# Performance work log

Hardware: AMD Instinct MI355X
Metric: run time of the kernel (lower is better)

The kernel has to match this reference:

```python
import jax, jax.numpy as jnp
import numpy as np


def setup_inputs() -> dict:
    key = jax.random.key(0)
    k1, k2 = jax.random.split(key)
    hidden_states = jax.random.normal(k1, (4, 4096, 2048), dtype=jnp.float32)
    routing_params = jax.random.normal(k2, (3, 2048), dtype=jnp.float32)
    return {"hidden_states": hidden_states, "routing_params": routing_params}


def reference(hidden_states, routing_params):
    B, S, H = hidden_states.shape
    D = routing_params.shape[0]  # max_recursion_depth
    k = max(1, int(S * (1.0 / D)))  # top-k tokens selected per step

    depth_assignments = jnp.zeros((B, S), dtype=jnp.int32)
    active_mask = jnp.ones((B, S), dtype=bool)
    rows = jnp.arange(B)[:, None]  # [B,1] row indices for scatter
    scores_list = []

    for r in range(D):  # small fixed depth loop
        raw = jnp.einsum('bsh,h->bs', hidden_states, routing_params[r])
        sc = jax.nn.sigmoid(raw)
        scores_list.append(sc)
        masked = jnp.where(active_mask, sc, -jnp.inf)
        _, top_idx = jax.lax.top_k(masked, k)  # [B,k]
        depth_assignments = depth_assignments.at[rows, top_idx].set(r + 1)
        step_mask = jnp.zeros((B, S), dtype=bool).at[rows, top_idx].set(True)
        active_mask = active_mask & step_mask

    depth_assignments = jnp.where(depth_assignments == 0, 1, depth_assignments)

    # balancing loss: note the original applies sigmoid AGAIN to the already-sigmoided scores
    probs = jax.nn.sigmoid(jnp.stack(scores_list, axis=-1)).mean(axis=(0, 1))  # [D]
    target = jnp.ones_like(probs) / D
    # F.kl_div(probs.log(), target, reduction='batchmean') with input of size D
    balancing_loss = jnp.sum(target * (jnp.log(target) - jnp.log(probs))) / D

    masks = jnp.stack([jnp.ones_like(active_mask) if r == 0 else active_mask
                       for r in range(D)])  # [D,B,S] bool
    return depth_assignments, balancing_loss, masks
```

## Files before the change

kernel.cpp:

```cpp
#include <hip/hip_runtime.h>
#include <math.h>

namespace {
constexpr int B = 4;
constexpr int S = 4096;
constexpr int H = 2048;
constexpr int DR = 3;
constexpr int KSEL = 1365;
constexpr int NBLK1 = 2048;
constexpr unsigned FONE = 0x3F800000u;
}

__global__ __launch_bounds__(256) void ecr_scores(const float* __restrict__ hid,
                                                  const float* __restrict__ w,
                                                  unsigned* __restrict__ keys,
                                                  float* __restrict__ partials,
                                                  float* __restrict__ out) {
    __shared__ float wl[DR * H];
    __shared__ float s2l[4][DR];
    const float4* wg4 = reinterpret_cast<const float4*>(w);
    float4* wl4 = reinterpret_cast<float4*>(wl);
    for (int i = threadIdx.x; i < DR * H / 4; i += 256) wl4[i] = wg4[i];
    __syncthreads();

    const int wave = threadIdx.x >> 6;
    const int lane = threadIdx.x & 63;
    const int gw = blockIdx.x * 4 + wave;
    const int t0 = gw * 2;
    const float4* wl4_0 = reinterpret_cast<const float4*>(wl);
    const float4* wl4_1 = wl4_0 + (H / 4);
    const float4* wl4_2 = wl4_0 + 2 * (H / 4);
    const float4* h40 = reinterpret_cast<const float4*>(hid) + (size_t)t0 * (H / 4);
    const float4* h41 = h40 + (H / 4);

    float a00 = 0.f, a01 = 0.f, a02 = 0.f;
    float a10 = 0.f, a11 = 0.f, a12 = 0.f;
#pragma unroll
    for (int j = 0; j < 8; ++j) {
        const int idx = j * 64 + lane;
        const float4 hv0 = h40[idx];
        const float4 hv1 = h41[idx];
        const float4 w0 = wl4_0[idx];
        const float4 w1 = wl4_1[idx];
        const float4 w2 = wl4_2[idx];
        a00 = fmaf(hv0.x, w0.x, a00); a10 = fmaf(hv1.x, w0.x, a10);
        a00 = fmaf(hv0.y, w0.y, a00); a10 = fmaf(hv1.y, w0.y, a10);
        a00 = fmaf(hv0.z, w0.z, a00); a10 = fmaf(hv1.z, w0.z, a10);
        a00 = fmaf(hv0.w, w0.w, a00); a10 = fmaf(hv1.w, w0.w, a10);
        a01 = fmaf(hv0.x, w1.x, a01); a11 = fmaf(hv1.x, w1.x, a11);
        a01 = fmaf(hv0.y, w1.y, a01); a11 = fmaf(hv1.y, w1.y, a11);
        a01 = fmaf(hv0.z, w1.z, a01); a11 = fmaf(hv1.z, w1.z, a11);
        a01 = fmaf(hv0.w, w1.w, a01); a11 = fmaf(hv1.w, w1.w, a11);
        a02 = fmaf(hv0.x, w2.x, a02); a12 = fmaf(hv1.x, w2.x, a12);
        a02 = fmaf(hv0.y, w2.y, a02); a12 = fmaf(hv1.y, w2.y, a12);
        a02 = fmaf(hv0.z, w2.z, a02); a12 = fmaf(hv1.z, w2.z, a12);
        a02 = fmaf(hv0.w, w2.w, a02); a12 = fmaf(hv1.w, w2.w, a12);
    }
#pragma unroll
    for (int off = 32; off >= 1; off >>= 1) {
        a00 += __shfl_xor(a00, off); a01 += __shfl_xor(a01, off);
        a02 += __shfl_xor(a02, off); a10 += __shfl_xor(a10, off);
        a11 += __shfl_xor(a11, off); a12 += __shfl_xor(a12, off);
    }
    if (lane == 0) {
        const float s00 = 1.0f / (1.0f + expf(-a00));
        const float s01 = 1.0f / (1.0f + expf(-a01));
        const float s02 = 1.0f / (1.0f + expf(-a02));
        const float s10 = 1.0f / (1.0f + expf(-a10));
        const float s11 = 1.0f / (1.0f + expf(-a11));
        const float s12 = 1.0f / (1.0f + expf(-a12));
        uint2 kk;
        kk.x = __float_as_uint(s00);
        kk.y = __float_as_uint(s10);
        *reinterpret_cast<uint2*>(keys + t0) = kk;
        s2l[wave][0] = 1.0f / (1.0f + expf(-s00)) + 1.0f / (1.0f + expf(-s10));
        s2l[wave][1] = 1.0f / (1.0f + expf(-s01)) + 1.0f / (1.0f + expf(-s11));
        s2l[wave][2] = 1.0f / (1.0f + expf(-s02)) + 1.0f / (1.0f + expf(-s12));
    }
    __syncthreads();
    if (threadIdx.x == 0) {
        float p0 = 0.f, p1 = 0.f, p2 = 0.f;
#pragma unroll
        for (int v = 0; v < 4; ++v) { p0 += s2l[v][0]; p1 += s2l[v][1]; p2 += s2l[v][2]; }
        partials[0 * NBLK1 + blockIdx.x] = p0;
        partials[1 * NBLK1 + blockIdx.x] = p1;
        partials[2 * NBLK1 + blockIdx.x] = p2;
    }
    if (threadIdx.x < 8)
        out[B * S + 1 + blockIdx.x * 8 + threadIdx.x] = 1.0f;
}

__global__ __launch_bounds__(512) void ecr_select(const unsigned* __restrict__ keys,
                                                  const float* __restrict__ partials,
                                                  float* __restrict__ out) {
    const int b = blockIdx.x;
    const int t = threadIdx.x;
    const int wave = t >> 6;
    const int lane = t & 63;

    __shared__ int wsum[2][8];
    __shared__ int wscan[8];

    unsigned kr[8];
#pragma unroll
    for (int i = 0; i < 8; ++i) kr[i] = keys[b * S + i * 512 + t];

    int c = 0;
#pragma unroll
    for (int i = 0; i < 8; ++i) c += (kr[i] == FONE);
#pragma unroll
    for (int off = 32; off >= 1; off >>= 1) c += __shfl_xor(c, off);
    if (lane == 0) wsum[0][wave] = c;
    __syncthreads();
    int tot1 = 0;
#pragma unroll
    for (int w2 = 0; w2 < 8; ++w2) tot1 += wsum[0][w2];

    unsigned vstar;
    int m;
    if (tot1 >= KSEL) {
        vstar = FONE;
        m = KSEL;
    } else {
        unsigned v = 0;
        int pb = 1;
        for (int bit = 29; bit >= 0; --bit) {
            const unsigned cand = v | (1u << bit);
            int cc = 0;
#pragma unroll
            for (int i = 0; i < 8; ++i) cc += (kr[i] >= cand);
#pragma unroll
            for (int off = 32; off >= 1; off >>= 1) cc += __shfl_xor(cc, off);
            if (lane == 0) wsum[pb][wave] = cc;
            __syncthreads();
            int tot = 0;
#pragma unroll
            for (int w2 = 0; w2 < 8; ++w2) tot += wsum[pb][w2];
            if (tot >= KSEL) v = cand;
            pb ^= 1;
        }
        vstar = v;
        int cg = 0;
#pragma unroll
        for (int i = 0; i < 8; ++i) cg += (kr[i] > vstar);
#pragma unroll
        for (int off = 32; off >= 1; off >>= 1) cg += __shfl_xor(cg, off);
        if (lane == 0) wsum[pb][wave] = cg;
        __syncthreads();
        int g = 0;
#pragma unroll
        for (int w2 = 0; w2 < 8; ++w2) g += wsum[pb][w2];
        m = KSEL - g;
    }
    __syncthreads();

    int rank[8];
    int cum = 0;
    for (int i = 0; i < 8; ++i) {
        const int tci = (kr[i] == vstar) ? 1 : 0;
        int sc = tci;
#pragma unroll
        for (int off = 1; off <= 32; off <<= 1) {
            const int o = __shfl_up(sc, off);
            if (lane >= off) sc += o;
        }
        if (lane == 63) wscan[wave] = sc;
        __syncthreads();
        int base = 0, tot = 0;
#pragma unroll
        for (int w2 = 0; w2 < 8; ++w2) {
            if (w2 < wave) base += wscan[w2];
            tot += wscan[w2];
        }
        rank[i] = cum + base + (sc - tci);
        cum += tot;
        __syncthreads();
    }

    float* depth  = out;
    float* masks1 = out + B * S + 1 + 1 * B * S;
    float* masks2 = out + B * S + 1 + 2 * B * S;
    const int s0 = b * S + t;
#pragma unroll
    for (int i = 0; i < 8; ++i) {
        int sel;
        if (kr[i] > vstar) sel = 1;
        else if (kr[i] == vstar) sel = (rank[i] < m) ? 1 : 0;
        else sel = 0;
        const float fsel = sel ? 1.0f : 0.0f;
        depth[s0 + i * 512]  = sel ? 3.0f : 1.0f;
        masks1[s0 + i * 512] = fsel;
        masks2[s0 + i * 512] = fsel;
    }

    if (b == 0) {
        __shared__ double red[3][8];
        const float4* p4 = reinterpret_cast<const float4*>(partials);
        const float4 v0 = p4[t];
        const float4 v1 = p4[NBLK1 / 4 + t];
        const float4 v2 = p4[NBLK1 / 2 + t];
        double a0 = (double)v0.x + (double)v0.y + (double)v0.z + (double)v0.w;
        double a1 = (double)v1.x + (double)v1.y + (double)v1.z + (double)v1.w;
        double a2 = (double)v2.x + (double)v2.y + (double)v2.z + (double)v2.w;
#pragma unroll
        for (int off = 32; off >= 1; off >>= 1) {
            a0 += __shfl_xor(a0, off);
            a1 += __shfl_xor(a1, off);
            a2 += __shfl_xor(a2, off);
        }
        if (lane == 0) { red[0][wave] = a0; red[1][wave] = a1; red[2][wave] = a2; }
        __syncthreads();
        if (t == 0) {
            double s0d = 0.0, s1d = 0.0, s2d = 0.0;
#pragma unroll
            for (int w2 = 0; w2 < 8; ++w2) { s0d += red[0][w2]; s1d += red[1][w2]; s2d += red[2][w2]; }
            const double n = (double)(B * S);
            const double lt = log(1.0 / 3.0);
            double l = (lt - log(s0d / n)) + (lt - log(s1d / n)) + (lt - log(s2d / n));
            out[B * S] = (float)(l * (1.0 / 3.0) / 3.0);
        }
    }
}

extern "C" void kernel_launch(void* const* d_in, const int* in_sizes, int n_in,
                              void* d_out, int out_size, void* d_ws, size_t ws_size,
                              hipStream_t stream) {
    const float* hid = (const float*)d_in[0];
    const float* w   = (const float*)d_in[1];
    float* out = (float*)d_out;

    unsigned* keys  = (unsigned*)d_ws;
    float* partials = (float*)((char*)d_ws + (size_t)B * S * sizeof(unsigned));

    ecr_scores<<<NBLK1, 256, 0, stream>>>(hid, w, keys, partials, out);
    ecr_select<<<B, 512, 0, stream>>>(keys, partials, out);
}
```

Before: 37.01 us.

## Split top-k select across 8 blocks per batch row with redundant threshold search

```diff
diff --git a/kernel.cpp b/kernel.cpp
--- a/kernel.cpp
+++ b/kernel.cpp
@@ -90,31 +90,42 @@
         out[B * S + 1 + blockIdx.x * 8 + threadIdx.x] = 1.0f;
 }
 
-__global__ __launch_bounds__(512) void ecr_select(const unsigned* __restrict__ keys,
+__global__ __launch_bounds__(256) void ecr_select(const unsigned* __restrict__ keys,
                                                   const float* __restrict__ partials,
                                                   float* __restrict__ out) {
-    const int b = blockIdx.x;
+    const int g = blockIdx.x;
+    const int b = g >> 3;
+    const int j = g & 7;
     const int t = threadIdx.x;
     const int wave = t >> 6;
     const int lane = t & 63;
 
-    __shared__ int wsum[2][8];
-    __shared__ int wscan[8];
-
-    unsigned kr[8];
-#pragma unroll
-    for (int i = 0; i < 8; ++i) kr[i] = keys[b * S + i * 512 + t];
+    __shared__ int wsum[2][4];
+    __shared__ int cred[4];
+    __shared__ int sA[4], sB[4];
+
+    const uint4* kp = reinterpret_cast<const uint4*>(keys + b * S);
+    unsigned kr[16];
+    int u4idx[4];
+#pragma unroll
+    for (int q = 0; q < 4; ++q) {
+        const int ui = t + 256 * q;
+        u4idx[q] = ui;
+        const uint4 v = kp[ui];
+        kr[4 * q + 0] = v.x; kr[4 * q + 1] = v.y;
+        kr[4 * q + 2] = v.z; kr[4 * q + 3] = v.w;
+    }
 
     int c = 0;
 #pragma unroll
-    for (int i = 0; i < 8; ++i) c += (kr[i] == FONE);
+    for (int i = 0; i < 16; ++i) c += (kr[i] == FONE);
 #pragma unroll
     for (int off = 32; off >= 1; off >>= 1) c += __shfl_xor(c, off);
     if (lane == 0) wsum[0][wave] = c;
     __syncthreads();
     int tot1 = 0;
 #pragma unroll
-    for (int w2 = 0; w2 < 8; ++w2) tot1 += wsum[0][w2];
+    for (int w2 = 0; w2 < 4; ++w2) tot1 += wsum[0][w2];
 
     unsigned vstar;
     int m;
@@ -128,80 +139,98 @@
             const unsigned cand = v | (1u << bit);
             int cc = 0;
 #pragma unroll
-            for (int i = 0; i < 8; ++i) cc += (kr[i] >= cand);
+            for (int i = 0; i < 16; ++i) cc += (kr[i] >= cand);
 #pragma unroll
             for (int off = 32; off >= 1; off >>= 1) cc += __shfl_xor(cc, off);
             if (lane == 0) wsum[pb][wave] = cc;
             __syncthreads();
             int tot = 0;
 #pragma unroll
-            for (int w2 = 0; w2 < 8; ++w2) tot += wsum[pb][w2];
+            for (int w2 = 0; w2 < 4; ++w2) tot += wsum[pb][w2];
             if (tot >= KSEL) v = cand;
             pb ^= 1;
         }
         vstar = v;
         int cg = 0;
 #pragma unroll
-        for (int i = 0; i < 8; ++i) cg += (kr[i] > vstar);
+        for (int i = 0; i < 16; ++i) cg += (kr[i] > vstar);
 #pragma unroll
         for (int off = 32; off >= 1; off >>= 1) cg += __shfl_xor(cg, off);
         if (lane == 0) wsum[pb][wave] = cg;
         __syncthreads();
-        int g = 0;
-#pragma unroll
-        for (int w2 = 0; w2 < 8; ++w2) g += wsum[pb][w2];
-        m = KSEL - g;
-    }
-    __syncthreads();
-
-    int rank[8];
+        int g2 = 0;
+#pragma unroll
+        for (int w2 = 0; w2 < 4; ++w2) g2 += wsum[pb][w2];
+        m = KSEL - g2;
+    }
+    __syncthreads();
+
+    int pc = 0;
+#pragma unroll
+    for (int q = 0; q < 4; ++q) {
+        if (u4idx[q] < j * 128) {
+#pragma unroll
+            for (int cidx = 0; cidx < 4; ++cidx) pc += (kr[4 * q + cidx] == vstar);
+        }
+    }
+#pragma unroll
+    for (int off = 32; off >= 1; off >>= 1) pc += __shfl_xor(pc, off);
+    if (lane == 0) cred[wave] = pc;
+    __syncthreads();
     int cum = 0;
-    for (int i = 0; i < 8; ++i) {
-        const int tci = (kr[i] == vstar) ? 1 : 0;
-        int sc = tci;
-#pragma unroll
-        for (int off = 1; off <= 32; off <<= 1) {
-            const int o = __shfl_up(sc, off);
-            if (lane >= off) sc += o;
-        }
-        if (lane == 63) wscan[wave] = sc;
-        __syncthreads();
-        int base = 0, tot = 0;
-#pragma unroll
-        for (int w2 = 0; w2 < 8; ++w2) {
-            if (w2 < wave) base += wscan[w2];
-            tot += wscan[w2];
-        }
-        rank[i] = cum + base + (sc - tci);
-        cum += tot;
-        __syncthreads();
-    }
-
+#pragma unroll
+    for (int w2 = 0; w2 < 4; ++w2) cum += cred[w2];
+
+    const int ia = b * S + j * 512 + t;
+    const unsigned ka = keys[ia];
+    const unsigned kb = keys[ia + 256];
+    const int fa = (ka == vstar) ? 1 : 0;
+    const int fb = (kb == vstar) ? 1 : 0;
+
+    int sa = fa, sb = fb;
+#pragma unroll
+    for (int off = 1; off <= 32; off <<= 1) {
+        const int oa = __shfl_up(sa, off);
+        const int ob = __shfl_up(sb, off);
+        if (lane >= off) { sa += oa; sb += ob; }
+    }
+    if (lane == 63) { sA[wave] = sa; sB[wave] = sb; }
+    __syncthreads();
+    int baseA = 0, totA = 0, baseB = 0;
+#pragma unroll
+    for (int w2 = 0; w2 < 4; ++w2) {
+        if (w2 < wave) { baseA += sA[w2]; baseB += sB[w2]; }
+        totA += sA[w2];
+    }
+    const int rank_a = cum + baseA + (sa - fa);
+    const int rank_b = cum + totA + baseB + (sb - fb);
+
+    const int sel_a = (ka > vstar) ? 1 : ((ka == vstar) ? (rank_a < m ? 1 : 0) : 0);
+    const int sel_b = (kb > vstar) ? 1 : ((kb == vstar) ? (rank_b < m ? 1 : 0) : 0);
     float* depth  = out;
     float* masks1 = out + B * S + 1 + 1 * B * S;
     float* masks2 = out + B * S + 1 + 2 * B * S;
-    const int s0 = b * S + t;
-#pragma unroll
-    for (int i = 0; i < 8; ++i) {
-        int sel;
-        if (kr[i] > vstar) sel = 1;
-        else if (kr[i] == vstar) sel = (rank[i] < m) ? 1 : 0;
-        else sel = 0;
-        const float fsel = sel ? 1.0f : 0.0f;
-        depth[s0 + i * 512]  = sel ? 3.0f : 1.0f;
-        masks1[s0 + i * 512] = fsel;
-        masks2[s0 + i * 512] = fsel;
-    }
-
-    if (b == 0) {
-        __shared__ double red[3][8];
+    depth[ia]        = sel_a ? 3.0f : 1.0f;
+    depth[ia + 256]  = sel_b ? 3.0f : 1.0f;
+    const float fsa = sel_a ? 1.0f : 0.0f;
+    const float fsb = sel_b ? 1.0f : 0.0f;
+    masks1[ia]       = fsa;
+    masks1[ia + 256] = fsb;
+    masks2[ia]       = fsa;
+    masks2[ia + 256] = fsb;
+
+    if (g == 0) {
+        __shared__ double red[3][4];
         const float4* p4 = reinterpret_cast<const float4*>(partials);
-        const float4 v0 = p4[t];
-        const float4 v1 = p4[NBLK1 / 4 + t];
-        const float4 v2 = p4[NBLK1 / 2 + t];
-        double a0 = (double)v0.x + (double)v0.y + (double)v0.z + (double)v0.w;
-        double a1 = (double)v1.x + (double)v1.y + (double)v1.z + (double)v1.w;
-        double a2 = (double)v2.x + (double)v2.y + (double)v2.z + (double)v2.w;
+        double a0 = 0.0, a1 = 0.0, a2 = 0.0;
+        for (int i = t; i < NBLK1 / 4; i += 256) {
+            const float4 v0 = p4[i];
+            const float4 v1 = p4[NBLK1 / 4 + i];
+            const float4 v2 = p4[NBLK1 / 2 + i];
+            a0 += (double)v0.x + (double)v0.y + (double)v0.z + (double)v0.w;
+            a1 += (double)v1.x + (double)v1.y + (double)v1.z + (double)v1.w;
+            a2 += (double)v2.x + (double)v2.y + (double)v2.z + (double)v2.w;
+        }
 #pragma unroll
         for (int off = 32; off >= 1; off >>= 1) {
             a0 += __shfl_xor(a0, off);
@@ -213,7 +242,7 @@
         if (t == 0) {
             double s0d = 0.0, s1d = 0.0, s2d = 0.0;
 #pragma unroll
-            for (int w2 = 0; w2 < 8; ++w2) { s0d += red[0][w2]; s1d += red[1][w2]; s2d += red[2][w2]; }
+            for (int w2 = 0; w2 < 4; ++w2) { s0d += red[0][w2]; s1d += red[1][w2]; s2d += red[2][w2]; }
             const double n = (double)(B * S);
             const double lt = log(1.0 / 3.0);
             double l = (lt - log(s0d / n)) + (lt - log(s1d / n)) + (lt - log(s2d / n));
@@ -233,5 +262,5 @@
     float* partials = (float*)((char*)d_ws + (size_t)B * S * sizeof(unsigned));
 
     ecr_scores<<<NBLK1, 256, 0, stream>>>(hid, w, keys, partials, out);
-    ecr_select<<<B, 512, 0, stream>>>(keys, partials, out);
-}
+    ecr_select<<<B * 8, 256, 0, stream>>>(keys, partials, out);
+}
```

Measured after the change: 34.81 us. -5.9%, faster.
